# Kernel tuning notes

Measured on AMD Instinct MI355X. Metric: run time of the kernel, lower is better.

The kernel has to match this reference:

```python
import jax, jax.numpy as jnp
import numpy as np

M = 4096   # output_features (sparse weight rows)
K = 4096   # input_features  (sparse weight cols)
B = 8
S = 2048
DENSITY = 0.1
NNZ = int(DENSITY * M * K)  # 1677721...


def setup_inputs() -> dict:
    key = jax.random.key(0)
    k1, k2, k3, k4, k5 = jax.random.split(key, 5)
    x = jax.random.normal(k1, (B, S, K), dtype=jnp.float32)
    values = jax.random.normal(k2, (1677722,), dtype=jnp.float32)
    bias = jax.random.normal(k3, (S,), dtype=jnp.float32)
    row_ids = jnp.sort(jax.random.randint(k4, (1677722,), 0, M, dtype=jnp.int32))
    column_indices = jax.random.randint(k5, (1677722,), 0, K, dtype=jnp.int32)
    return {"x": x, "values": values, "bias": bias,
            "row_ids": row_ids, "column_indices": column_indices}


def reference(x, values, bias, row_ids, column_indices):
    # Sparse weight W[m,k] in COO (CSR rows expanded to row_ids); duplicates accumulate.
    W = jnp.zeros((M, K), dtype=values.dtype).at[row_ids, column_indices].add(values)
    # left_spmm: W[m,k] @ x^T[b,k,s] -> [b,m,s], then + bias (broadcast over last dim)
    out = jnp.einsum('mk,bsk->bms', W, x) + bias  # bias shape [S] broadcasts on last axis
    return out
```

## Files before the change

kernel.cpp:

```cpp
#include <hip/hip_runtime.h>
#include <hip/hip_bf16.h>
#include <stdint.h>


#define M_DIM 4096
#define K_DIM 4096
#define B_DIM 8
#define S_DIM 2048

#define BM 128
#define BN 128
#define BK 64

typedef float  f32x4  __attribute__((ext_vector_type(4)));
typedef __bf16 bf16x8 __attribute__((ext_vector_type(8)));

__device__ __forceinline__ uint32_t f32_bits(float f){ union{float f;uint32_t u;} v; v.f=f; return v.u; }
__device__ __forceinline__ uint16_t f2bf(float f){
  uint32_t u = f32_bits(f);
  uint32_t r = u + 0x7FFFu + ((u >> 16) & 1u);
  return (uint16_t)(r >> 16);
}


__global__ void scatter_kernel(const float* __restrict__ vals,
                               const int* __restrict__ rows,
                               const int* __restrict__ cols,
                               float* __restrict__ W, int nnz){
  int i = blockIdx.x * 256 + threadIdx.x;
  if (i < nnz) atomicAdd(W + (size_t)rows[i] * K_DIM + cols[i], vals[i]);
}

__global__ void cvt_kernel(const float* __restrict__ in,
                           uint16_t* __restrict__ out, int n4){
  int i = blockIdx.x * 256 + threadIdx.x;
  if (i >= n4) return;
  float4 w = ((const float4*)in)[i];
  ushort4 h;
  h.x = f2bf(w.x); h.y = f2bf(w.y); h.z = f2bf(w.z); h.w = f2bf(w.w);
  ((ushort4*)out)[i] = h;
}


__global__ __launch_bounds__(256, 2) void gemm_bf16(
    const uint16_t* __restrict__ Wbf, const uint16_t* __restrict__ Xbf,
    const float* __restrict__ bias, float* __restrict__ out)
{
  __shared__ uint16_t lA[BM * BK];
  __shared__ uint16_t lB[BN * BK];

  const int tid  = threadIdx.x;
  const int lane = tid & 63;
  const int wid  = tid >> 6;
  const int wm   = (wid >> 1) * 64;
  const int wn   = (wid & 1) * 64;
  const int l15  = lane & 15;
  const int l4   = lane >> 4;

  const int bid = blockIdx.x;
  const int wg  = (bid & 7) * 512 + (bid >> 3);
  const int b   = wg >> 9;
  const int rem = wg & 511;
  const int m0  = (rem >> 4) * BM;
  const int s0  = (rem & 15) * BN;

  const uint16_t* __restrict__ Bb = Xbf + (size_t)b * S_DIM * K_DIM;

  f32x4 acc[4][4] = {};

  for (int kt = 0; kt < K_DIM / BK; ++kt) {
    const int k0 = kt * BK;
    __syncthreads();

    #pragma unroll
    for (int i = 0; i < 4; ++i) {
      int idx = i * 256 + tid;
      int r = idx >> 3;
      int c = (idx & 7) * 8;
      const uint16_t* gp = Wbf + (size_t)(m0 + r) * K_DIM + (k0 + c);
      __builtin_amdgcn_global_load_lds(
          (const __attribute__((address_space(1))) void*)gp,
          (__attribute__((address_space(3))) void*)(&lA[idx * 8]), 16, 0, 0);
    }
    #pragma unroll
    for (int i = 0; i < 4; ++i) {
      int idx = i * 256 + tid;
      int r = idx >> 3;
      int c = (idx & 7) * 8;
      const uint16_t* gp = Bb + (size_t)(s0 + r) * K_DIM + (k0 + c);
      __builtin_amdgcn_global_load_lds(
          (const __attribute__((address_space(1))) void*)gp,
          (__attribute__((address_space(3))) void*)(&lB[idx * 8]), 16, 0, 0);
    }
    __syncthreads();

    #pragma unroll
    for (int ks = 0; ks < 2; ++ks) {
      bf16x8 af[4], bfr[4];
      #pragma unroll
      for (int mi = 0; mi < 4; ++mi)
        af[mi] = *(const bf16x8*)&lA[(wm + mi * 16 + l15) * BK + ks * 32 + l4 * 8];
      #pragma unroll
      for (int ni = 0; ni < 4; ++ni)
        bfr[ni] = *(const bf16x8*)&lB[(wn + ni * 16 + l15) * BK + ks * 32 + l4 * 8];
      #pragma unroll
      for (int mi = 0; mi < 4; ++mi)
        #pragma unroll
        for (int ni = 0; ni < 4; ++ni)
          acc[mi][ni] = __builtin_amdgcn_mfma_f32_16x16x32_bf16(
              af[mi], bfr[ni], acc[mi][ni], 0, 0, 0);
    }
  }

  #pragma unroll
  for (int ni = 0; ni < 4; ++ni) {
    const int scol = wn + ni * 16 + l15;
    const float bv = bias[s0 + scol];
    #pragma unroll
    for (int mi = 0; mi < 4; ++mi) {
      const int rbase = wm + mi * 16 + l4 * 4;
      float* op = out + ((size_t)b * M_DIM + m0 + rbase) * S_DIM + s0 + scol;
      #pragma unroll
      for (int r = 0; r < 4; ++r)
        op[(size_t)r * S_DIM] = acc[mi][ni][r] + bv;
    }
  }
}


extern "C" void kernel_launch(void* const* d_in, const int* in_sizes, int n_in,
                              void* d_out, int out_size, void* d_ws, size_t ws_size,
                              hipStream_t stream) {
  const float* x       = (const float*)d_in[0];
  const float* values  = (const float*)d_in[1];
  const float* bias    = (const float*)d_in[2];
  const int*   row_ids = (const int*)d_in[3];
  const int*   col_idx = (const int*)d_in[4];
  const int    nnz     = in_sizes[1];
  float*       out     = (float*)d_out;

  char* ws = (char*)d_ws;
  float*    W32 = (float*)ws;
  uint16_t* Wbf = (uint16_t*)(ws + (size_t)64 * 1024 * 1024);
  uint16_t* Xbf = (uint16_t*)(ws + (size_t)96 * 1024 * 1024);

  hipMemsetAsync(W32, 0, (size_t)M_DIM * K_DIM * sizeof(float), stream);
  scatter_kernel<<<(nnz + 255) / 256, 256, 0, stream>>>(values, row_ids, col_idx, W32, nnz);

  const int nW4 = M_DIM * K_DIM / 4;
  cvt_kernel<<<(nW4 + 255) / 256, 256, 0, stream>>>(W32, Wbf, nW4);
  const int nX4 = B_DIM * S_DIM * K_DIM / 4;
  cvt_kernel<<<(nX4 + 255) / 256, 256, 0, stream>>>(x, Xbf, nX4);

  dim3 grid(M_DIM / BM * (S_DIM / BN) * B_DIM);
  gemm_bf16<<<grid, 256, 0, stream>>>(Wbf, Xbf, bias, out);
}
```

Before: 1.064 ms.

## Rewrite GEMM as 256x256 tile, 8-wave, 8-phase double-buffered pipeline

Replaces the 128x128 single-buffered bf16 GEMM with a 256x256 tile run by 8 waves and 512 threads. LDS is double-buffered with half-tile staging, interleaved across 8 phases so global-to-LDS loads overlap MFMA work. The LDS layout uses an XOR swizzle to avoid bank conflicts, and s_setprio is raised around MFMA bursts. The larger tile improves data reuse. The cost is more LDS (128KB per block) and more registers, which lowers occupancy, and the explicit vmcnt and barrier schedule is fragile.

```diff
diff --git a/kernel.cpp b/kernel.cpp
--- a/kernel.cpp
+++ b/kernel.cpp
@@ -7,10 +7,6 @@
 #define K_DIM 4096
 #define B_DIM 8
 #define S_DIM 2048
-
-#define BM 128
-#define BN 128
-#define BK 64
 
 typedef float  f32x4  __attribute__((ext_vector_type(4)));
 typedef __bf16 bf16x8 __attribute__((ext_vector_type(8)));
@@ -42,87 +38,137 @@
 }
 
 
-__global__ __launch_bounds__(256, 2) void gemm_bf16(
+__device__ __forceinline__ void stage_half(
+    uint16_t* ldsbase, const uint16_t* gbase,
+    int row0, int interleaveA, int h, int k0, int tid)
+{
+  #pragma unroll
+  for (int j = 0; j < 2; ++j) {
+    int c  = j * 512 + tid;
+    int cs = c ^ (((c >> 5) & 1) << 1);
+    int rp  = cs >> 3;
+    int col = (cs & 7) << 3;
+    int gr;
+    if (interleaveA) gr = 64 * h + (rp & 63) + ((rp >> 6) << 7);
+    else             gr = rp + (h << 7);
+    const uint16_t* gp = gbase + (size_t)(row0 + gr) * K_DIM + (k0 + col);
+    __builtin_amdgcn_global_load_lds(
+        (const __attribute__((address_space(1))) void*)gp,
+        (__attribute__((address_space(3))) void*)(ldsbase + c * 8), 16, 0, 0);
+  }
+}
+
+__global__ __launch_bounds__(512, 2) void gemm_8ph(
     const uint16_t* __restrict__ Wbf, const uint16_t* __restrict__ Xbf,
     const float* __restrict__ bias, float* __restrict__ out)
 {
-  __shared__ uint16_t lA[BM * BK];
-  __shared__ uint16_t lB[BN * BK];
+  __shared__ uint16_t lds[2][2][2][8192];
 
   const int tid  = threadIdx.x;
   const int lane = tid & 63;
   const int wid  = tid >> 6;
-  const int wm   = (wid >> 1) * 64;
-  const int wn   = (wid & 1) * 64;
+  const int wr   = wid >> 2;
+  const int wc   = wid & 3;
   const int l15  = lane & 15;
   const int l4   = lane >> 4;
 
   const int bid = blockIdx.x;
-  const int wg  = (bid & 7) * 512 + (bid >> 3);
-  const int b   = wg >> 9;
-  const int rem = wg & 511;
-  const int m0  = (rem >> 4) * BM;
-  const int s0  = (rem & 15) * BN;
-
-  const uint16_t* __restrict__ Bb = Xbf + (size_t)b * S_DIM * K_DIM;
-
-  f32x4 acc[4][4] = {};
-
-  for (int kt = 0; kt < K_DIM / BK; ++kt) {
-    const int k0 = kt * BK;
-    __syncthreads();
+  const int wg  = (bid & 7) * 128 + (bid >> 3);
+  const int b   = wg >> 7;
+  const int rem = wg & 127;
+  const int m0  = (rem >> 3) * 256;
+  const int s0  = (rem & 7) * 256;
+
+  const uint16_t* Xb = Xbf + (size_t)b * S_DIM * K_DIM;
+
+  f32x4 acc[8][4] = {};
+
+  stage_half(&lds[0][1][0][0], Xb,  s0, 0, 0, 0,  tid);
+  stage_half(&lds[0][1][1][0], Xb,  s0, 0, 1, 0,  tid);
+  stage_half(&lds[0][0][0][0], Wbf, m0, 1, 0, 0,  tid);
+  stage_half(&lds[0][0][1][0], Wbf, m0, 1, 1, 0,  tid);
+  stage_half(&lds[1][1][0][0], Xb,  s0, 0, 0, 64, tid);
+  stage_half(&lds[1][1][1][0], Xb,  s0, 0, 1, 64, tid);
+  stage_half(&lds[1][0][0][0], Wbf, m0, 1, 0, 64, tid);
+  asm volatile("s_waitcnt vmcnt(6)" ::: "memory");
+  __builtin_amdgcn_s_barrier();
+  __builtin_amdgcn_sched_barrier(0);
+
+  for (int it = 0; it < K_DIM / 128; ++it) {
+    const int kt1 = it * 128 + 64;
+    const int kn0 = (it * 128 + 128) & (K_DIM - 1);
+    const int kn1 = (it * 128 + 192) & (K_DIM - 1);
+    bf16x8 bfr[4][2];
 
     #pragma unroll
-    for (int i = 0; i < 4; ++i) {
-      int idx = i * 256 + tid;
-      int r = idx >> 3;
-      int c = (idx & 7) * 8;
-      const uint16_t* gp = Wbf + (size_t)(m0 + r) * K_DIM + (k0 + c);
-      __builtin_amdgcn_global_load_lds(
-          (const __attribute__((address_space(1))) void*)gp,
-          (__attribute__((address_space(3))) void*)(&lA[idx * 8]), 16, 0, 0);
-    }
-    #pragma unroll
-    for (int i = 0; i < 4; ++i) {
-      int idx = i * 256 + tid;
-      int r = idx >> 3;
-      int c = (idx & 7) * 8;
-      const uint16_t* gp = Bb + (size_t)(s0 + r) * K_DIM + (k0 + c);
-      __builtin_amdgcn_global_load_lds(
-          (const __attribute__((address_space(1))) void*)gp,
-          (__attribute__((address_space(3))) void*)(&lB[idx * 8]), 16, 0, 0);
-    }
-    __syncthreads();
-
-    #pragma unroll
-    for (int ks = 0; ks < 2; ++ks) {
-      bf16x8 af[4], bfr[4];
-      #pragma unroll
-      for (int mi = 0; mi < 4; ++mi)
-        af[mi] = *(const bf16x8*)&lA[(wm + mi * 16 + l15) * BK + ks * 32 + l4 * 8];
-      #pragma unroll
-      for (int ni = 0; ni < 4; ++ni)
-        bfr[ni] = *(const bf16x8*)&lB[(wn + ni * 16 + l15) * BK + ks * 32 + l4 * 8];
-      #pragma unroll
-      for (int mi = 0; mi < 4; ++mi)
+    for (int ph = 0; ph < 8; ++ph) {
+      const int buf = ph >> 2;
+      const int q   = ph & 3;
+
+      if (q == 0) {
         #pragma unroll
         for (int ni = 0; ni < 4; ++ni)
-          acc[mi][ni] = __builtin_amdgcn_mfma_f32_16x16x32_bf16(
-              af[mi], bfr[ni], acc[mi][ni], 0, 0, 0);
+          #pragma unroll
+          for (int ks = 0; ks < 2; ++ks) {
+            int idx = ((wc & 1) * 64 + ni * 16 + l15) * 64 + ks * 32 + l4 * 8;
+            idx ^= ((idx >> 8) & 1) << 4;
+            bfr[ni][ks] = *(const bf16x8*)&lds[buf][1][wc >> 1][idx];
+          }
+      }
+      bf16x8 af[2][2];
+      #pragma unroll
+      for (int mi = 0; mi < 2; ++mi)
+        #pragma unroll
+        for (int ks = 0; ks < 2; ++ks) {
+          int idx = (wr * 64 + (q & 1) * 32 + mi * 16 + l15) * 64 + ks * 32 + l4 * 8;
+          idx ^= ((idx >> 8) & 1) << 4;
+          af[mi][ks] = *(const bf16x8*)&lds[buf][0][q >> 1][idx];
+        }
+
+      switch (ph) {
+        case 0: stage_half(&lds[1][0][1][0], Wbf, m0, 1, 1, kt1, tid); break;
+        case 1: stage_half(&lds[0][1][0][0], Xb,  s0, 0, 0, kn0, tid); break;
+        case 2: stage_half(&lds[0][1][1][0], Xb,  s0, 0, 1, kn0, tid); break;
+        case 3: stage_half(&lds[0][0][0][0], Wbf, m0, 1, 0, kn0, tid); break;
+        case 4: stage_half(&lds[0][0][1][0], Wbf, m0, 1, 1, kn0, tid); break;
+        case 5: stage_half(&lds[1][1][0][0], Xb,  s0, 0, 0, kn1, tid); break;
+        case 6: stage_half(&lds[1][1][1][0], Xb,  s0, 0, 1, kn1, tid); break;
+        case 7: stage_half(&lds[1][0][0][0], Wbf, m0, 1, 0, kn1, tid); break;
+      }
+      if (q == 3) asm volatile("s_waitcnt vmcnt(6)" ::: "memory");
+
+      __builtin_amdgcn_s_barrier();
+      __builtin_amdgcn_sched_barrier(0);
+      asm volatile("s_waitcnt lgkmcnt(0)" ::: "memory");
+      __builtin_amdgcn_sched_barrier(0);
+
+      __builtin_amdgcn_s_setprio(1);
+      #pragma unroll
+      for (int mi = 0; mi < 2; ++mi)
+        #pragma unroll
+        for (int ni = 0; ni < 4; ++ni)
+          #pragma unroll
+          for (int ks = 0; ks < 2; ++ks)
+            acc[q * 2 + mi][ni] = __builtin_amdgcn_mfma_f32_16x16x32_bf16(
+                af[mi][ks], bfr[ni][ks], acc[q * 2 + mi][ni], 0, 0, 0);
+      __builtin_amdgcn_s_setprio(0);
+
+      __builtin_amdgcn_s_barrier();
+      __builtin_amdgcn_sched_barrier(0);
     }
   }
 
   #pragma unroll
   for (int ni = 0; ni < 4; ++ni) {
-    const int scol = wn + ni * 16 + l15;
-    const float bv = bias[s0 + scol];
+    const int scol = s0 + wc * 64 + ni * 16 + l15;
+    const float bv = bias[scol];
     #pragma unroll
-    for (int mi = 0; mi < 4; ++mi) {
-      const int rbase = wm + mi * 16 + l4 * 4;
-      float* op = out + ((size_t)b * M_DIM + m0 + rbase) * S_DIM + s0 + scol;
+    for (int am = 0; am < 8; ++am) {
+      const int mrow = m0 + wr * 128 + am * 16 + l4 * 4;
+      float* op = out + ((size_t)b * M_DIM + mrow) * S_DIM + scol;
       #pragma unroll
       for (int r = 0; r < 4; ++r)
-        op[(size_t)r * S_DIM] = acc[mi][ni][r] + bv;
+        op[(size_t)r * S_DIM] = acc[am][ni][r] + bv;
     }
   }
 }
@@ -152,6 +198,6 @@
   const int nX4 = B_DIM * S_DIM * K_DIM / 4;
   cvt_kernel<<<(nX4 + 255) / 256, 256, 0, stream>>>(x, Xbf, nX4);
 
-  dim3 grid(M_DIM / BM * (S_DIM / BN) * B_DIM);
-  gemm_bf16<<<grid, 256, 0, stream>>>(Wbf, Xbf, bias, out);
-}
+  dim3 grid(M_DIM / 256 * (S_DIM / 256) * B_DIM);
+  gemm_8ph<<<grid, 512, 0, stream>>>(Wbf, Xbf, bias, out);
+}
```

After: 986.3 us. 7.3% less time.
